# Kernel optimization log

Measured on AMD Instinct MI355X. Metric: run time of the kernel, lower is better.

## Reference

```python
import math
import jax, jax.numpy as jnp
import numpy as np

B, N, D, NC, TMAX = 8, 4096, 1024, 512, 1000


def setup_inputs() -> dict:
    key = jax.random.key(0)
    ks = jax.random.split(key, 12)
    tokens = jax.random.normal(ks[0], (B, N, D), jnp.float32)
    ctx_C = jax.random.normal(ks[1], (B, NC, D), jnp.float32)
    t = jax.random.randint(ks[2], (B,), 0, TMAX, dtype=jnp.int32)
    rare_mask = jax.random.bernoulli(ks[3], 0.05, (B, N))
    # Linear params stored as (in, out); scaled so scores straddle 0.5
    ctx_w = jax.random.normal(ks[4], (D, D // 4), jnp.float32) / math.sqrt(D)
    ctx_b = jax.random.normal(ks[5], (D // 4,), jnp.float32) * 0.01
    t_proj_w = jax.random.normal(ks[6], (D, D), jnp.float32) / math.sqrt(D)
    t_proj_b = jax.random.normal(ks[7], (D,), jnp.float32) * 0.01
    HIN = D + D // 4 + D  # 2304
    w1 = jax.random.normal(ks[8], (HIN, D // 2), jnp.float32) / math.sqrt(HIN)
    b1 = jax.random.normal(ks[9], (D // 2,), jnp.float32) * 0.01
    w2 = jax.random.normal(ks[10], (D // 2,), jnp.float32) * 0.1
    b2 = jnp.zeros((1,), jnp.float32)
    return {"tokens": tokens, "ctx_C": ctx_C, "t": t, "rare_mask": rare_mask,
            "ctx_w": ctx_w, "ctx_b": ctx_b, "t_proj_w": t_proj_w,
            "t_proj_b": t_proj_b, "w1": w1, "b1": b1, "w2": w2, "b2": b2}


def reference(tokens, ctx_C, t, rare_mask, ctx_w, ctx_b, t_proj_w, t_proj_b, w1, b1, w2, b2):
    Bb, Nn, Dd = tokens.shape
    half = Dd // 2
    # sinusoidal timestep embedding buffer (matches torch register_buffer)
    freq = jnp.exp(-math.log(10000.0) * jnp.arange(half, dtype=jnp.float32) / max(half - 1, 1))
    # bottlenecked context: mean over ctx tokens -> (B, D//4)
    ctx_bn = ctx_C.mean(axis=1) @ ctx_w + ctx_b
    args = t.astype(jnp.float32)[:, None] * freq[None, :]            # (B, half)
    emb = jnp.concatenate([jnp.sin(args), jnp.cos(args)], axis=-1)   # (B, D)
    t_emb = emb @ t_proj_w + t_proj_b                                # (B, D)
    x = jnp.concatenate([
        tokens,
        jnp.broadcast_to(ctx_bn[:, None, :], (Bb, Nn, Dd // 4)),
        jnp.broadcast_to(t_emb[:, None, :], (Bb, Nn, Dd)),
    ], axis=-1)                                                       # (B, N, 2.25D)
    h = jax.nn.relu(x @ w1 + b1)                                      # (B, N, D//2)
    scores = jax.nn.sigmoid(h @ w2 + b2)                              # (B, N)
    skip = (scores > 0.5) & jnp.logical_not(rare_mask)
    min_active = max(1, int(Nn * 0.2))
    active = jnp.logical_not(skip).sum(axis=-1)                       # (B,)
    deficit = jnp.maximum(min_active - active, 0)                     # (B,)
    masked = jnp.where(skip, scores, jnp.inf)
    rank = jnp.argsort(jnp.argsort(masked, axis=-1), axis=-1)         # rank among skipped, ascending score
    skip = skip & jnp.logical_not(rank < deficit[:, None])
    return skip, scores
```

## Files before the change

kernel.cpp:

```cpp
#include <hip/hip_runtime.h>
#include <math.h>

#define NN 4096
#define DD 1024
#define M_TOT 32768
#define H1 512
#define MIN_ACTIVE 819
#define MARGIN 0.03f
#define MAXFIX 8192

typedef __bf16 bf16x8 __attribute__((ext_vector_type(8)));
typedef float f32x4 __attribute__((ext_vector_type(4)));

__device__ __forceinline__ unsigned short f2bf(float f) {
    unsigned int u = __float_as_uint(f);
    return (unsigned short)((u + 0x7FFFu + ((u >> 16) & 1u)) >> 16);
}

__device__ __forceinline__ void glds16(const unsigned short* g, unsigned short* l) {
    __builtin_amdgcn_global_load_lds(
        (const __attribute__((address_space(1))) unsigned int*)g,
        (__attribute__((address_space(3))) unsigned int*)l, 16, 0, 0);
}

__global__ void convB_pmean_kernel(const float* __restrict__ w1, unsigned short* __restrict__ w1tt,
                                   const float* __restrict__ ctx, float* __restrict__ pmean,
                                   const unsigned char* __restrict__ rare, int* __restrict__ mode,
                                   int* __restrict__ fixcnt) {
    __shared__ float tile[32][65];
    __shared__ int nonbin, oneoff;
    int blk = blockIdx.x;
    int tid = threadIdx.x;
    if (blk < 256) {
        int t = blk >> 3;
        int c0 = (blk & 7) * 64;
        #pragma unroll
        for (int i = 0; i < 8; ++i) {
            int idx = tid + 256 * i;
            int kk = idx >> 6, cc = idx & 63;
            tile[kk][cc] = w1[(size_t)(t * 32 + kk) * H1 + c0 + cc];
        }
        __syncthreads();
        {
            int cc = tid >> 2, jp = tid & 3;
            int c = c0 + cc;
            int j = jp ^ ((c >> 1) & 3);
            unsigned int w[4];
            #pragma unroll
            for (int q = 0; q < 4; ++q)
                w[q] = (unsigned int)f2bf(tile[j * 8 + 2 * q][cc])
                     | ((unsigned int)f2bf(tile[j * 8 + 2 * q + 1][cc]) << 16);
            uint4 v; v.x = w[0]; v.y = w[1]; v.z = w[2]; v.w = w[3];
            *(uint4*)(w1tt + ((size_t)t * 512 + c) * 32 + jp * 8) = v;
        }
        if (blk == 0) {
            if (tid == 0) { nonbin = 0; oneoff = 0; *fixcnt = 0; }
            __syncthreads();
            int lnon = 0, lone = 0;
            for (int i = tid; i < 32768; i += 256) {
                unsigned char b = rare[i];
                if (b > 1) lnon = 1;
                else if (b == 1 && (i & 3) != 0) lone = 1;
            }
            if (lnon) atomicOr(&nonbin, 1);
            if (lone) atomicOr(&oneoff, 1);
            __syncthreads();
            if (tid == 0) *mode = nonbin ? 2 : (oneoff ? 1 : 0);
        }
    } else {
        int pblk = blk - 256;
        int b = pblk >> 5, dq = (pblk >> 3) & 3, nz = pblk & 7;
        int d = dq * 256 + tid;
        const float* base = ctx + ((size_t)(b * 512 + nz * 64)) * DD + d;
        float acc = 0.f;
        for (int n = 0; n < 64; ++n) acc += base[(size_t)n * DD];
        pmean[(b * 8 + nz) * DD + d] = acc;
    }
}

__global__ void prep_kernel(const float* __restrict__ pmean, const int* __restrict__ t,
                            float* __restrict__ mean, float* __restrict__ embf) {
    int idx = blockIdx.x * 256 + threadIdx.x;
    int b = idx >> 10, j = idx & 1023;
    float s = 0.f;
    for (int nz = 0; nz < 8; ++nz) s += pmean[(b * 8 + nz) * DD + j];
    mean[idx] = s * (1.f / 512.f);
    int jj = j & 511;
    double arg = (double)t[b] * exp((-log(10000.0) / 511.0) * (double)jj);
    embf[idx] = (float)((j < 512) ? sin(arg) : cos(arg));
}

__global__ __launch_bounds__(256) void midk_kernel(
    const float* __restrict__ mean, const float* __restrict__ embf,
    const float* __restrict__ ctx_w, const float* __restrict__ ctx_b,
    const float* __restrict__ tpw, const float* __restrict__ tpb,
    float* __restrict__ ctx_bn, float* __restrict__ t_emb) {
    __shared__ float red8[8][32];
    __shared__ float red4[4][64];
    int tid = threadIdx.x;
    if (blockIdx.x < 64) {
        int b = blockIdx.x >> 3, cg = blockIdx.x & 7;
        int c = cg * 32 + (tid & 31), ks = tid >> 5;
        const float* mb = mean + b * DD + ks * 128;
        const float* wb = ctx_w + (size_t)(ks * 128) * 256 + c;
        float acc = 0.f;
        for (int i = 0; i < 128; ++i) acc += mb[i] * wb[(size_t)i * 256];
        red8[ks][tid & 31] = acc;
        __syncthreads();
        if (tid < 32) {
            float s = 0.f;
            for (int k = 0; k < 8; ++k) s += red8[k][tid];
            ctx_bn[b * 256 + cg * 32 + tid] = s + ctx_b[cg * 32 + tid];
        }
    } else {
        int blk = blockIdx.x - 64;
        int b = blk >> 4, cg = blk & 15;
        int c = cg * 64 + (tid & 63), ks = tid >> 6;
        const float* eb = embf + b * DD + ks * 256;
        const float* wb = tpw + (size_t)(ks * 256) * DD + c;
        float acc = 0.f;
        for (int i = 0; i < 256; ++i) acc += eb[i] * wb[(size_t)i * DD];
        red4[ks][tid & 63] = acc;
        __syncthreads();
        if (tid < 64) {
            float s = red4[0][tid] + red4[1][tid] + red4[2][tid] + red4[3][tid];
            t_emb[b * DD + cg * 64 + tid] = s + tpb[cg * 64 + tid];
        }
    }
}

__global__ void baseh_kernel(const float* __restrict__ ctx_bn, const float* __restrict__ t_emb,
                             const float* __restrict__ w1, const float* __restrict__ b1,
                             float* __restrict__ base_h) {
    __shared__ float red[8][32];
    int b = blockIdx.x, cg = blockIdx.y;
    int c = cg * 32 + (threadIdx.x & 31), ks = threadIdx.x >> 5;
    float acc = 0.f;
    for (int i = 0; i < 160; ++i) {
        int k = ks * 160 + i;
        float v = (k < 256) ? ctx_bn[b * 256 + k] : t_emb[b * DD + k - 256];
        acc += v * w1[(size_t)(1024 + k) * H1 + c];
    }
    red[ks][threadIdx.x & 31] = acc;
    __syncthreads();
    if (threadIdx.x < 32) {
        float s = 0.f;
        for (int k = 0; k < 8; ++k) s += red[k][threadIdx.x];
        base_h[b * H1 + cg * 32 + threadIdx.x] = s + b1[cg * 32 + threadIdx.x];
    }
}

__global__ __launch_bounds__(512, 4) void gemm_kernel(
    const float* __restrict__ tokens, const unsigned short* __restrict__ w1tt,
    const float* __restrict__ baseh, const float* __restrict__ w2,
    float* __restrict__ part) {
    __shared__ unsigned short As[2][128 * 40];
    __shared__ unsigned short Bs[3][256 * 32];
    __shared__ float red[128][4];
    int tid = threadIdx.x;
    int lane = tid & 63, wid = tid >> 6;
    int wm = wid >> 2, wn = wid & 3;
    int la = lane & 15, lk = lane >> 4;
    int row0 = blockIdx.x * 128;
    int half = blockIdx.y;
    const unsigned short* wsrc = w1tt + (size_t)half * 256 * 32;

    f32x4 acc[4][4];
    #pragma unroll
    for (int i = 0; i < 4; ++i)
        #pragma unroll
        for (int j = 0; j < 4; ++j)
            acc[i][j] = (f32x4){0.f, 0.f, 0.f, 0.f};

    float4 sa0[2], sa1[2];
    #define LOAD_A(kt_, S_) { \
        _Pragma("unroll") \
        for (int i = 0; i < 2; ++i) { \
            int id = tid + 512 * i; \
            int r = id >> 3, xk = id & 7; \
            S_[i] = *(const float4*)(tokens + (size_t)(row0 + r) * DD + (kt_) + xk * 4); \
        } }
    #define WRITE_A(bb_, S_) { \
        _Pragma("unroll") \
        for (int i = 0; i < 2; ++i) { \
            int id = tid + 512 * i; \
            int r = id >> 3, xk = id & 7; \
            ushort4 h; \
            h.x = f2bf(S_[i].x); h.y = f2bf(S_[i].y); \
            h.z = f2bf(S_[i].z); h.w = f2bf(S_[i].w); \
            *(ushort4*)(&As[bb_][r * 40 + xk * 4]) = h; \
        } }
    #define STAGE_B(t_, bb_) { \
        const unsigned short* gsrc = wsrc + (size_t)(t_) * 512 * 32; \
        _Pragma("unroll") \
        for (int q = 0; q < 2; ++q) { \
            int chunk = wid * 2 + q; \
            glds16(gsrc + chunk * 512 + lane * 8, &Bs[bb_][chunk * 512]); \
        } }

    LOAD_A(0, sa0);
    STAGE_B(0, 0);
    STAGE_B(1, 1);
    WRITE_A(0, sa0);
    LOAD_A(32, sa1);
    __builtin_amdgcn_sched_barrier(0);
    asm volatile("s_waitcnt vmcnt(4)" ::: "memory");
    asm volatile("s_waitcnt lgkmcnt(0)" ::: "memory");
    __builtin_amdgcn_s_barrier();
    __builtin_amdgcn_sched_barrier(0);

    for (int t = 0; t < 32; ++t) {
        int bb = t & 1;
        const unsigned short* bsrc = Bs[t % 3];
        bf16x8 af[4], bfr[4];
        #pragma unroll
        for (int mf = 0; mf < 4; ++mf) {
            int r = wm * 64 + mf * 16 + la;
            af[mf] = *(const bf16x8*)(&As[bb][r * 40 + lk * 8]);
        }
        #pragma unroll
        for (int nf = 0; nf < 4; ++nf) {
            int c = wn * 64 + nf * 16 + la;
            int sw = lk ^ ((c >> 1) & 3);
            bfr[nf] = *(const bf16x8*)(&bsrc[c * 32 + sw * 8]);
        }
        __builtin_amdgcn_s_setprio(1);
        #pragma unroll
        for (int mf = 0; mf < 4; ++mf)
            #pragma unroll
            for (int nf = 0; nf < 4; ++nf)
                acc[mf][nf] = __builtin_amdgcn_mfma_f32_16x16x32_bf16(af[mf], bfr[nf], acc[mf][nf], 0, 0, 0);
        __builtin_amdgcn_s_setprio(0);
        __builtin_amdgcn_sched_barrier(0);
        if (t < 31) {
            if (t & 1) { WRITE_A(bb ^ 1, sa0) } else { WRITE_A(bb ^ 1, sa1) }
            if (t < 30) {
                if (t & 1) { LOAD_A((t + 2) * 32, sa1) } else { LOAD_A((t + 2) * 32, sa0) }
                STAGE_B(t + 2, (t + 2) % 3);
            }
            __builtin_amdgcn_sched_barrier(0);
            if (t < 30) asm volatile("s_waitcnt vmcnt(4)" ::: "memory");
            else        asm volatile("s_waitcnt vmcnt(0)" ::: "memory");
            asm volatile("s_waitcnt lgkmcnt(0)" ::: "memory");
            __builtin_amdgcn_s_barrier();
            __builtin_amdgcn_sched_barrier(0);
        }
    }
    #undef LOAD_A
    #undef WRITE_A
    #undef STAGE_B

    int b = row0 >> 12;
    const float* bh = baseh + b * H1;
    float bhv[4], w2v[4];
    #pragma unroll
    for (int nf = 0; nf < 4; ++nf) {
        int col = half * 256 + wn * 64 + nf * 16 + la;
        bhv[nf] = bh[col];
        w2v[nf] = w2[col];
    }
    #pragma unroll
    for (int mf = 0; mf < 4; ++mf) {
        #pragma unroll
        for (int reg = 0; reg < 4; ++reg) {
            float p = 0.f;
            #pragma unroll
            for (int nf = 0; nf < 4; ++nf) {
                float h = acc[mf][nf][reg] + bhv[nf];
                h = fmaxf(h, 0.f);
                p += h * w2v[nf];
            }
            p += __shfl_xor(p, 1, 64);
            p += __shfl_xor(p, 2, 64);
            p += __shfl_xor(p, 4, 64);
            p += __shfl_xor(p, 8, 64);
            if (la == 0) red[wm * 64 + mf * 16 + lk * 4 + reg][wn] = p;
        }
    }
    __syncthreads();
    if (tid < 128)
        part[(size_t)(row0 + tid) * 2 + half] = red[tid][0] + red[tid][1] + red[tid][2] + red[tid][3];
}

__global__ void score_kernel(const float* __restrict__ part, const float* __restrict__ b2,
                             const void* __restrict__ rare, const int* __restrict__ mode_p,
                             float* __restrict__ out, int* __restrict__ fixcnt,
                             int* __restrict__ fixlist) {
    int row = blockIdx.x * 256 + threadIdx.x;
    float logit = part[(size_t)row * 2] + part[(size_t)row * 2 + 1] + b2[0];
    float score = 1.f / (1.f + expf(-logit));
    int mode = *mode_p;
    bool rm = (mode == 1) ? (((const unsigned char*)rare)[row] != 0)
            : (mode == 2) ? (((const float*)rare)[row] != 0.f)
            : (((const int*)rare)[row] != 0);
    out[row] = ((score > 0.5f) && !rm) ? 1.f : 0.f;
    out[M_TOT + row] = score;
    if (fabsf(logit) < MARGIN) {
        int i = atomicAdd(fixcnt, 1);
        if (i < MAXFIX) fixlist[i] = row;
    }
}

__global__ __launch_bounds__(512) void fixup_kernel(
    const int* __restrict__ fixcnt, const int* __restrict__ fixlist,
    const float* __restrict__ tokens, const float* __restrict__ w1,
    const float* __restrict__ base_h, const float* __restrict__ w2,
    const float* __restrict__ b2, const void* __restrict__ rare,
    const int* __restrict__ mode_p, float* __restrict__ out) {
    __shared__ float tok[DD];
    __shared__ float part4[4][H1];
    __shared__ float red[8];
    int tid = threadIdx.x;
    int lane = tid & 63, wid = tid >> 6;
    int ks = tid >> 7;
    int cg = tid & 127;
    int n = *fixcnt;
    if (n > MAXFIX) n = MAXFIX;
    for (int g = blockIdx.x; g < n; g += gridDim.x) {
        int row = fixlist[g];
        int b = row >> 12;
        if (tid < 256)
            ((float4*)tok)[tid] = ((const float4*)(tokens + (size_t)row * DD))[tid];
        __syncthreads();
        const float* wbase = w1 + (size_t)(ks * 256) * H1 + cg * 4;
        const float* tbase = tok + ks * 256;
        float4 a = {0.f, 0.f, 0.f, 0.f};
        #pragma unroll 8
        for (int k = 0; k < 256; ++k) {
            float4 w = *(const float4*)(wbase + (size_t)k * H1);
            float tv = tbase[k];
            a.x += tv * w.x; a.y += tv * w.y; a.z += tv * w.z; a.w += tv * w.w;
        }
        *(float4*)&part4[ks][cg * 4] = a;
        __syncthreads();
        float h = part4[0][tid] + part4[1][tid] + part4[2][tid] + part4[3][tid]
                + base_h[b * H1 + tid];
        h = fmaxf(h, 0.f);
        float p = h * w2[tid];
        p += __shfl_xor(p, 1, 64);
        p += __shfl_xor(p, 2, 64);
        p += __shfl_xor(p, 4, 64);
        p += __shfl_xor(p, 8, 64);
        p += __shfl_xor(p, 16, 64);
        p += __shfl_xor(p, 32, 64);
        if (lane == 0) red[wid] = p;
        __syncthreads();
        if (tid == 0) {
            float logit = b2[0];
            #pragma unroll
            for (int w = 0; w < 8; ++w) logit += red[w];
            float score = 1.f / (1.f + expf(-logit));
            int mode = *mode_p;
            bool rm = (mode == 1) ? (((const unsigned char*)rare)[row] != 0)
                    : (mode == 2) ? (((const float*)rare)[row] != 0.f)
                    : (((const int*)rare)[row] != 0);
            out[row] = ((score > 0.5f) && !rm) ? 1.f : 0.f;
            out[M_TOT + row] = score;
        }
        __syncthreads();
    }
}

__global__ void floor_kernel(float* __restrict__ out) {
    __shared__ float s[NN];
    __shared__ unsigned char f[NN];
    __shared__ int cnt;
    int b = blockIdx.x, tid = threadIdx.x;
    if (tid == 0) cnt = 0;
    __syncthreads();
    int local = 0;
    for (int i = tid; i < NN; i += 256) {
        s[i] = out[M_TOT + b * NN + i];
        unsigned char sk = out[b * NN + i] > 0.5f;
        f[i] = sk;
        local += sk;
    }
    atomicAdd(&cnt, local);
    __syncthreads();
    int deficit = cnt - (NN - MIN_ACTIVE);
    if (deficit <= 0) return;
    for (int i = tid; i < NN; i += 256) {
        if (!f[i]) continue;
        float si = s[i];
        int rank = 0;
        for (int j = 0; j < NN; ++j) {
            if (f[j] && (s[j] < si || (s[j] == si && j < i))) {
                if (++rank >= deficit) break;
            }
        }
        if (rank < deficit) out[b * NN + i] = 0.f;
    }
}

extern "C" void kernel_launch(void* const* d_in, const int* in_sizes, int n_in,
                              void* d_out, int out_size, void* d_ws, size_t ws_size,
                              hipStream_t stream) {
    const float* tokens   = (const float*)d_in[0];
    const float* ctx_C    = (const float*)d_in[1];
    const int*   t        = (const int*)d_in[2];
    const void*  rare     = d_in[3];
    const float* ctx_w    = (const float*)d_in[4];
    const float* ctx_b    = (const float*)d_in[5];
    const float* t_proj_w = (const float*)d_in[6];
    const float* t_proj_b = (const float*)d_in[7];
    const float* w1       = (const float*)d_in[8];
    const float* b1       = (const float*)d_in[9];
    const float* w2       = (const float*)d_in[10];
    const float* b2       = (const float*)d_in[11];
    float* out = (float*)d_out;

    char* ws = (char*)d_ws;
    unsigned short* w1tt  = (unsigned short*)(ws);
    float* pmean          = (float*)(ws + 1048576);
    float* part           = (float*)(ws + 1048576);
    float* mean           = (float*)(ws + 1310720);
    float* embf           = (float*)(ws + 1343488);
    float* ctx_bn         = (float*)(ws + 1376256);
    float* t_emb          = (float*)(ws + 1384448);
    float* base_h         = (float*)(ws + 1417216);
    int*   mode           = (int*)  (ws + 1433600);
    int*   fixcnt         = (int*)  (ws + 1433664);
    int*   fixlist        = (int*)  (ws + 1433728);

    convB_pmean_kernel<<<512, 256, 0, stream>>>(w1, w1tt, ctx_C, pmean,
                                                (const unsigned char*)rare, mode, fixcnt);
    prep_kernel<<<32, 256, 0, stream>>>(pmean, t, mean, embf);
    midk_kernel<<<192, 256, 0, stream>>>(mean, embf, ctx_w, ctx_b, t_proj_w, t_proj_b, ctx_bn, t_emb);
    baseh_kernel<<<dim3(8, 16), 256, 0, stream>>>(ctx_bn, t_emb, w1, b1, base_h);
    gemm_kernel<<<dim3(256, 2), 512, 0, stream>>>(tokens, w1tt, base_h, w2, part);
    score_kernel<<<128, 256, 0, stream>>>(part, b2, rare, mode, out, fixcnt, fixlist);
    fixup_kernel<<<512, 512, 0, stream>>>(fixcnt, fixlist, tokens, w1, base_h, w2, b2, rare, mode, out);
    floor_kernel<<<8, 256, 0, stream>>>(out);
}
```

Measured before the change: 177.9 us.

## Fuse prep into midk, widen GEMM tile to full N, fold scoring into GEMM

Moves the context mean and sinusoidal embedding computation into midk_kernel's shared memory, removing prep_kernel and its intermediate buffers. The GEMM now has each block cover all 512 hidden columns instead of two halves, so the token tile is loaded and converted to bf16 once rather than twice. Because each block then holds the complete logit, score_kernel's sigmoid, mask and fixup-list logic runs in the GEMM epilogue and the partial-sum buffer goes away. The cost is twice the accumulator registers and LDS per block, half as many blocks (256), and lower occupancy (launch bounds 512,2).

```diff
diff --git a/kernel.cpp b/kernel.cpp
--- a/kernel.cpp
+++ b/kernel.cpp
@@ -78,30 +78,26 @@
     }
 }
 
-__global__ void prep_kernel(const float* __restrict__ pmean, const int* __restrict__ t,
-                            float* __restrict__ mean, float* __restrict__ embf) {
-    int idx = blockIdx.x * 256 + threadIdx.x;
-    int b = idx >> 10, j = idx & 1023;
-    float s = 0.f;
-    for (int nz = 0; nz < 8; ++nz) s += pmean[(b * 8 + nz) * DD + j];
-    mean[idx] = s * (1.f / 512.f);
-    int jj = j & 511;
-    double arg = (double)t[b] * exp((-log(10000.0) / 511.0) * (double)jj);
-    embf[idx] = (float)((j < 512) ? sin(arg) : cos(arg));
-}
-
 __global__ __launch_bounds__(256) void midk_kernel(
-    const float* __restrict__ mean, const float* __restrict__ embf,
+    const float* __restrict__ pmean, const int* __restrict__ t,
     const float* __restrict__ ctx_w, const float* __restrict__ ctx_b,
     const float* __restrict__ tpw, const float* __restrict__ tpb,
     float* __restrict__ ctx_bn, float* __restrict__ t_emb) {
+    __shared__ float sh[1024];
     __shared__ float red8[8][32];
     __shared__ float red4[4][64];
     int tid = threadIdx.x;
     if (blockIdx.x < 64) {
         int b = blockIdx.x >> 3, cg = blockIdx.x & 7;
+        for (int j = tid; j < 1024; j += 256) {
+            float s = 0.f;
+            #pragma unroll
+            for (int nz = 0; nz < 8; ++nz) s += pmean[(b * 8 + nz) * DD + j];
+            sh[j] = s * (1.f / 512.f);
+        }
+        __syncthreads();
         int c = cg * 32 + (tid & 31), ks = tid >> 5;
-        const float* mb = mean + b * DD + ks * 128;
+        const float* mb = sh + ks * 128;
         const float* wb = ctx_w + (size_t)(ks * 128) * 256 + c;
         float acc = 0.f;
         for (int i = 0; i < 128; ++i) acc += mb[i] * wb[(size_t)i * 256];
@@ -115,8 +111,16 @@
     } else {
         int blk = blockIdx.x - 64;
         int b = blk >> 4, cg = blk & 15;
+        double tv = (double)t[b];
+        const double neg_ln = -log(10000.0) / 511.0;
+        for (int j = tid; j < 1024; j += 256) {
+            int jj = j & 511;
+            double arg = tv * exp(neg_ln * (double)jj);
+            sh[j] = (float)((j < 512) ? sin(arg) : cos(arg));
+        }
+        __syncthreads();
         int c = cg * 64 + (tid & 63), ks = tid >> 6;
-        const float* eb = embf + b * DD + ks * 256;
+        const float* eb = sh + ks * 256;
         const float* wb = tpw + (size_t)(ks * 256) * DD + c;
         float acc = 0.f;
         for (int i = 0; i < 256; ++i) acc += eb[i] * wb[(size_t)i * DD];
@@ -150,26 +154,26 @@
     }
 }
 
-__global__ __launch_bounds__(512, 4) void gemm_kernel(
+__global__ __launch_bounds__(512, 2) void gemm_kernel(
     const float* __restrict__ tokens, const unsigned short* __restrict__ w1tt,
     const float* __restrict__ baseh, const float* __restrict__ w2,
-    float* __restrict__ part) {
+    const float* __restrict__ b2, const void* __restrict__ rare,
+    const int* __restrict__ mode_p, float* __restrict__ out,
+    int* __restrict__ fixcnt, int* __restrict__ fixlist) {
     __shared__ unsigned short As[2][128 * 40];
-    __shared__ unsigned short Bs[3][256 * 32];
+    __shared__ unsigned short Bs[3][512 * 32];
     __shared__ float red[128][4];
     int tid = threadIdx.x;
     int lane = tid & 63, wid = tid >> 6;
     int wm = wid >> 2, wn = wid & 3;
     int la = lane & 15, lk = lane >> 4;
     int row0 = blockIdx.x * 128;
-    int half = blockIdx.y;
-    const unsigned short* wsrc = w1tt + (size_t)half * 256 * 32;
-
-    f32x4 acc[4][4];
+
+    f32x4 acc[4][8];
     #pragma unroll
     for (int i = 0; i < 4; ++i)
         #pragma unroll
-        for (int j = 0; j < 4; ++j)
+        for (int j = 0; j < 8; ++j)
             acc[i][j] = (f32x4){0.f, 0.f, 0.f, 0.f};
 
     float4 sa0[2], sa1[2];
@@ -191,10 +195,10 @@
             *(ushort4*)(&As[bb_][r * 40 + xk * 4]) = h; \
         } }
     #define STAGE_B(t_, bb_) { \
-        const unsigned short* gsrc = wsrc + (size_t)(t_) * 512 * 32; \
+        const unsigned short* gsrc = w1tt + (size_t)(t_) * 512 * 32; \
         _Pragma("unroll") \
-        for (int q = 0; q < 2; ++q) { \
-            int chunk = wid * 2 + q; \
+        for (int q = 0; q < 4; ++q) { \
+            int chunk = wid * 4 + q; \
             glds16(gsrc + chunk * 512 + lane * 8, &Bs[bb_][chunk * 512]); \
         } }
 
@@ -204,7 +208,7 @@
     WRITE_A(0, sa0);
     LOAD_A(32, sa1);
     __builtin_amdgcn_sched_barrier(0);
-    asm volatile("s_waitcnt vmcnt(4)" ::: "memory");
+    asm volatile("s_waitcnt vmcnt(6)" ::: "memory");
     asm volatile("s_waitcnt lgkmcnt(0)" ::: "memory");
     __builtin_amdgcn_s_barrier();
     __builtin_amdgcn_sched_barrier(0);
@@ -212,15 +216,15 @@
     for (int t = 0; t < 32; ++t) {
         int bb = t & 1;
         const unsigned short* bsrc = Bs[t % 3];
-        bf16x8 af[4], bfr[4];
+        bf16x8 af[4], bfr[8];
         #pragma unroll
         for (int mf = 0; mf < 4; ++mf) {
             int r = wm * 64 + mf * 16 + la;
             af[mf] = *(const bf16x8*)(&As[bb][r * 40 + lk * 8]);
         }
         #pragma unroll
-        for (int nf = 0; nf < 4; ++nf) {
-            int c = wn * 64 + nf * 16 + la;
+        for (int nf = 0; nf < 8; ++nf) {
+            int c = wn * 128 + nf * 16 + la;
             int sw = lk ^ ((c >> 1) & 3);
             bfr[nf] = *(const bf16x8*)(&bsrc[c * 32 + sw * 8]);
         }
@@ -228,7 +232,7 @@
         #pragma unroll
         for (int mf = 0; mf < 4; ++mf)
             #pragma unroll
-            for (int nf = 0; nf < 4; ++nf)
+            for (int nf = 0; nf < 8; ++nf)
                 acc[mf][nf] = __builtin_amdgcn_mfma_f32_16x16x32_bf16(af[mf], bfr[nf], acc[mf][nf], 0, 0, 0);
         __builtin_amdgcn_s_setprio(0);
         __builtin_amdgcn_sched_barrier(0);
@@ -239,7 +243,7 @@
                 STAGE_B(t + 2, (t + 2) % 3);
             }
             __builtin_amdgcn_sched_barrier(0);
-            if (t < 30) asm volatile("s_waitcnt vmcnt(4)" ::: "memory");
+            if (t < 30) asm volatile("s_waitcnt vmcnt(6)" ::: "memory");
             else        asm volatile("s_waitcnt vmcnt(0)" ::: "memory");
             asm volatile("s_waitcnt lgkmcnt(0)" ::: "memory");
             __builtin_amdgcn_s_barrier();
@@ -252,10 +256,10 @@
 
     int b = row0 >> 12;
     const float* bh = baseh + b * H1;
-    float bhv[4], w2v[4];
+    float bhv[8], w2v[8];
     #pragma unroll
-    for (int nf = 0; nf < 4; ++nf) {
-        int col = half * 256 + wn * 64 + nf * 16 + la;
+    for (int nf = 0; nf < 8; ++nf) {
+        int col = wn * 128 + nf * 16 + la;
         bhv[nf] = bh[col];
         w2v[nf] = w2[col];
     }
@@ -265,7 +269,7 @@
         for (int reg = 0; reg < 4; ++reg) {
             float p = 0.f;
             #pragma unroll
-            for (int nf = 0; nf < 4; ++nf) {
+            for (int nf = 0; nf < 8; ++nf) {
                 float h = acc[mf][nf][reg] + bhv[nf];
                 h = fmaxf(h, 0.f);
                 p += h * w2v[nf];
@@ -278,26 +282,20 @@
         }
     }
     __syncthreads();
-    if (tid < 128)
-        part[(size_t)(row0 + tid) * 2 + half] = red[tid][0] + red[tid][1] + red[tid][2] + red[tid][3];
-}
-
-__global__ void score_kernel(const float* __restrict__ part, const float* __restrict__ b2,
-                             const void* __restrict__ rare, const int* __restrict__ mode_p,
-                             float* __restrict__ out, int* __restrict__ fixcnt,
-                             int* __restrict__ fixlist) {
-    int row = blockIdx.x * 256 + threadIdx.x;
-    float logit = part[(size_t)row * 2] + part[(size_t)row * 2 + 1] + b2[0];
-    float score = 1.f / (1.f + expf(-logit));
-    int mode = *mode_p;
-    bool rm = (mode == 1) ? (((const unsigned char*)rare)[row] != 0)
-            : (mode == 2) ? (((const float*)rare)[row] != 0.f)
-            : (((const int*)rare)[row] != 0);
-    out[row] = ((score > 0.5f) && !rm) ? 1.f : 0.f;
-    out[M_TOT + row] = score;
-    if (fabsf(logit) < MARGIN) {
-        int i = atomicAdd(fixcnt, 1);
-        if (i < MAXFIX) fixlist[i] = row;
+    if (tid < 128) {
+        int row = row0 + tid;
+        float logit = red[tid][0] + red[tid][1] + red[tid][2] + red[tid][3] + b2[0];
+        float score = 1.f / (1.f + expf(-logit));
+        int mode = *mode_p;
+        bool rm = (mode == 1) ? (((const unsigned char*)rare)[row] != 0)
+                : (mode == 2) ? (((const float*)rare)[row] != 0.f)
+                : (((const int*)rare)[row] != 0);
+        out[row] = ((score > 0.5f) && !rm) ? 1.f : 0.f;
+        out[M_TOT + row] = score;
+        if (fabsf(logit) < MARGIN) {
+            int i = atomicAdd(fixcnt, 1);
+            if (i < MAXFIX) fixlist[i] = row;
+        }
     }
 }
 
@@ -412,23 +410,18 @@
     char* ws = (char*)d_ws;
     unsigned short* w1tt  = (unsigned short*)(ws);
     float* pmean          = (float*)(ws + 1048576);
-    float* part           = (float*)(ws + 1048576);
-    float* mean           = (float*)(ws + 1310720);
-    float* embf           = (float*)(ws + 1343488);
-    float* ctx_bn         = (float*)(ws + 1376256);
-    float* t_emb          = (float*)(ws + 1384448);
-    float* base_h         = (float*)(ws + 1417216);
-    int*   mode           = (int*)  (ws + 1433600);
-    int*   fixcnt         = (int*)  (ws + 1433664);
-    int*   fixlist        = (int*)  (ws + 1433728);
+    float* ctx_bn         = (float*)(ws + 1310720);
+    float* t_emb          = (float*)(ws + 1318912);
+    float* base_h         = (float*)(ws + 1351680);
+    int*   mode           = (int*)  (ws + 1368064);
+    int*   fixcnt         = (int*)  (ws + 1368128);
+    int*   fixlist        = (int*)  (ws + 1368192);
 
     convB_pmean_kernel<<<512, 256, 0, stream>>>(w1, w1tt, ctx_C, pmean,
                                                 (const unsigned char*)rare, mode, fixcnt);
-    prep_kernel<<<32, 256, 0, stream>>>(pmean, t, mean, embf);
-    midk_kernel<<<192, 256, 0, stream>>>(mean, embf, ctx_w, ctx_b, t_proj_w, t_proj_b, ctx_bn, t_emb);
+    midk_kernel<<<192, 256, 0, stream>>>(pmean, t, ctx_w, ctx_b, t_proj_w, t_proj_b, ctx_bn, t_emb);
     baseh_kernel<<<dim3(8, 16), 256, 0, stream>>>(ctx_bn, t_emb, w1, b1, base_h);
-    gemm_kernel<<<dim3(256, 2), 512, 0, stream>>>(tokens, w1tt, base_h, w2, part);
-    score_kernel<<<128, 256, 0, stream>>>(part, b2, rare, mode, out, fixcnt, fixlist);
+    gemm_kernel<<<256, 512, 0, stream>>>(tokens, w1tt, base_h, w2, b2, rare, mode, out, fixcnt, fixlist);
     fixup_kernel<<<512, 512, 0, stream>>>(fixcnt, fixlist, tokens, w1, base_h, w2, b2, rare, mode, out);
     floor_kernel<<<8, 256, 0, stream>>>(out);
 }
```

Measured after the change: 179.7 us. No clear change (+1.0%).
